# Kernel tuning notes

Measured on AMD Instinct MI355X. Metric: run time of the kernel, lower is better.

The kernel has to match this reference:

```python
import jax, jax.numpy as jnp
import numpy as np

D_MODEL = 1024
NUM_HEADS = 16
D_HEAD = D_MODEL // NUM_HEADS
NEG_INF = float(np.finfo(np.float32).min)


def setup_inputs() -> dict:
    key = jax.random.key(0)
    ks = jax.random.split(key, 6)
    B, S = 2, 2048
    q = jax.random.normal(ks[0], (B, S, D_MODEL), dtype=jnp.float32)
    k = jax.random.normal(ks[1], (B, S, D_MODEL), dtype=jnp.float32)
    v = jax.random.normal(ks[2], (B, S, D_MODEL), dtype=jnp.float32)
    # causal boolean mask: True = attend
    attn_mask = jnp.tril(jnp.ones((S, S), dtype=bool))
    # nn.Linear(d_model, d_model, bias=False) weights: [out, in]; y = x @ W.T
    init_scale = 1.0 / np.sqrt(D_MODEL)
    Wq = jax.random.uniform(ks[3], (D_MODEL, D_MODEL), jnp.float32, -init_scale, init_scale)
    Wk = jax.random.uniform(ks[4], (D_MODEL, D_MODEL), jnp.float32, -init_scale, init_scale)
    Wv = jax.random.uniform(ks[5], (D_MODEL, D_MODEL), jnp.float32, -init_scale, init_scale)
    return {"query": q, "key": k, "value": v, "Wq": Wq, "Wk": Wk, "Wv": Wv,
            "attn_mask": attn_mask}


def _split_heads(x):
    # [B, S, D_MODEL] -> [B, H, S, d_head]
    B, S, _ = x.shape
    return x.reshape(B, S, NUM_HEADS, D_HEAD).transpose(0, 2, 1, 3)


def reference(query, key, value, Wq, Wk, Wv, attn_mask):
    B, Sq, _ = query.shape
    Sk = key.shape[1]
    q = _split_heads(query @ Wq.T)   # [B, H, Sq, dh]
    k = _split_heads(key @ Wk.T)     # [B, H, Sk, dh]
    v = _split_heads(value @ Wv.T)   # [B, H, Sk, dh]
    scale = 1.0 / np.sqrt(D_HEAD)
    scores = jnp.einsum('bhqd,bhkd->bhqk', q, k) * scale  # [B, H, Sq, Sk]
    scores = jnp.where(attn_mask[None, None, :, :], scores, NEG_INF)
    attn_weights = jax.nn.softmax(scores, axis=-1)
    ctx = jnp.einsum('bhqk,bhkd->bhqd', attn_weights, v)   # [B, H, Sq, dh]
    context = ctx.transpose(0, 2, 1, 3).reshape(B, Sq, D_MODEL)
    return context, attn_weights
```

## Files before the change

kernel.cpp:

```cpp
#include <hip/hip_runtime.h>
#include <hip/hip_bf16.h>

#define B_ 2
#define H_ 16
#define S_ 2048
#define DH_ 64
#define DM_ 1024
#define BH_ (B_*H_)
#define CTX_ELEMS (B_*S_*DM_)
#define ATTNW_ELEMS ((size_t)BH_*S_*S_)
#define OUT_ELEMS ((size_t)CTX_ELEMS + ATTNW_ELEMS)
#define HEAD_ELEMS (S_*DH_)
#define XB_ELEMS ((size_t)3*B_*S_*DM_)

typedef __attribute__((ext_vector_type(4))) float  f32x4;
typedef __attribute__((ext_vector_type(8))) short  short8;
typedef __attribute__((ext_vector_type(4))) unsigned short ush4;
typedef unsigned short u16;
typedef unsigned int u32;

__device__ __forceinline__ u16 f2bf(float f) {
  union { __hip_bfloat16 h; u16 u; } cv;
  cv.h = __float2bfloat16(f);
  return cv.u;
}
__device__ __forceinline__ float bf2f(u16 u) {
  union { unsigned int i; float f; } cv;
  cv.i = ((unsigned int)u) << 16;
  return cv.f;
}

__device__ __forceinline__ void gload_lds16(const u16* g, u16* l) {
  __builtin_amdgcn_global_load_lds(
      (const __attribute__((address_space(1))) u32*)g,
      (__attribute__((address_space(3))) u32*)l, 16, 0, 0);
}

__global__ __launch_bounds__(256) void convert_all(
    const float* __restrict__ q, const float* __restrict__ k, const float* __restrict__ v,
    const float* __restrict__ wq, const float* __restrict__ wk, const float* __restrict__ wv,
    u16* __restrict__ xb, u16* __restrict__ wb)
{
  const int t = blockIdx.y;
  const float* s; u16* d; int nblk;
  if (t < 3) {
    s = (t == 0) ? wq : (t == 1) ? wk : wv;
    d = wb + (size_t)t * (DM_ * DM_);
    nblk = 512;
  } else {
    s = (t == 3) ? q : (t == 4) ? k : v;
    d = xb + (size_t)(t - 3) * ((size_t)B_ * S_ * DM_);
    nblk = 2048;
  }
  if (blockIdx.x >= nblk) return;
  const int i = (blockIdx.x * 256 + threadIdx.x) * 8;
  f32x4 a = *(const f32x4*)(s + i);
  f32x4 b = *(const f32x4*)(s + i + 4);
  short8 p;
#pragma unroll
  for (int j = 0; j < 4; ++j) { p[j] = (short)f2bf(a[j]); p[4 + j] = (short)f2bf(b[j]); }
  *(short8*)(d + i) = p;
}

__global__ __launch_bounds__(256) void proj_gemm(
    const u16* __restrict__ Xb, const u16* __restrict__ Wb,
    u16* __restrict__ qb, u16* __restrict__ kb, u16* __restrict__ vt,
    float* __restrict__ attnw)
{
  const u16* A = Xb + (size_t)blockIdx.z * ((size_t)B_ * S_ * DM_);
  const u16* W = Wb + (size_t)blockIdx.z * (DM_ * DM_);

  const int m0 = blockIdx.x * 128;
  const int n0 = blockIdx.y * 128;

  __shared__ u16 As[128 * 32];
  __shared__ u16 Bs[128 * 32];

  const int tid  = threadIdx.x;
  const int lane = tid & 63;
  const int w    = tid >> 6;
  const int wr   = w >> 1, wc = w & 1;
  const int l15  = lane & 15, l4 = lane >> 4;

  f32x4 acc[4][4];
#pragma unroll
  for (int i = 0; i < 4; ++i)
#pragma unroll
    for (int j = 0; j < 4; ++j) acc[i][j] = (f32x4){0.f, 0.f, 0.f, 0.f};

  const int srow = lane >> 2;
  const int scol = (lane & 3) * 8;
  const int ca = w * 2;
  const u16* ga0 = A + (size_t)(m0 + ca * 16 + srow) * DM_ + scol;
  const u16* ga1 = A + (size_t)(m0 + ca * 16 + 16 + srow) * DM_ + scol;
  const u16* gb0 = W + (size_t)(n0 + ca * 16 + srow) * DM_ + scol;
  const u16* gb1 = W + (size_t)(n0 + ca * 16 + 16 + srow) * DM_ + scol;

  for (int kb = 0; kb < DM_ / 32; ++kb) {
    const int k0 = kb * 32;
    gload_lds16(ga0 + k0, &As[ca * 512]);
    gload_lds16(ga1 + k0, &As[ca * 512 + 512]);
    gload_lds16(gb0 + k0, &Bs[ca * 512]);
    gload_lds16(gb1 + k0, &Bs[ca * 512 + 512]);
    __syncthreads();
    short8 af[4], bfr[4];
#pragma unroll
    for (int i = 0; i < 4; ++i)
      af[i] = *(const short8*)&As[(wr * 64 + i * 16 + l15) * 32 + l4 * 8];
#pragma unroll
    for (int j = 0; j < 4; ++j)
      bfr[j] = *(const short8*)&Bs[(wc * 64 + j * 16 + l15) * 32 + l4 * 8];
#pragma unroll
    for (int i = 0; i < 4; ++i)
#pragma unroll
      for (int j = 0; j < 4; ++j)
        acc[i][j] = __builtin_amdgcn_mfma_f32_16x16x32_bf16(af[i], bfr[j], acc[i][j], 0, 0, 0);
    __syncthreads();
  }

  if (blockIdx.z == 2) {
#pragma unroll
    for (int i = 0; i < 4; ++i)
#pragma unroll
      for (int j = 0; j < 4; ++j)
#pragma unroll
        for (int r = 0; r < 4; ++r) {
          const int grow = m0 + wr * 64 + i * 16 + l4 * 4 + r;
          const int gcol = n0 + wc * 64 + j * 16 + l15;
          const int b = grow >> 11, s = grow & (S_ - 1);
          const int h = gcol >> 6,  d = gcol & (DH_ - 1);
          vt[(size_t)((b << 4) + h) * HEAD_ELEMS + (size_t)d * S_ + s] = f2bf(acc[i][j][r]);
        }
  } else {
    u16* O = (blockIdx.z == 0) ? qb : kb;
#pragma unroll
    for (int i = 0; i < 4; ++i)
#pragma unroll
      for (int j = 0; j < 4; ++j)
#pragma unroll
        for (int r = 0; r < 4; ++r) {
          const int grow = m0 + wr * 64 + i * 16 + l4 * 4 + r;
          const int gcol = n0 + wc * 64 + j * 16 + l15;
          const int b = grow >> 11, s = grow & (S_ - 1);
          const int h = gcol >> 6,  d = gcol & (DH_ - 1);
          O[(size_t)((b << 4) + h) * HEAD_ELEMS + (size_t)s * DH_ + d] = f2bf(acc[i][j][r]);
        }
  }

  {
    const int p = (blockIdx.z * 8 + blockIdx.y) * 32 + blockIdx.x;
    const f32x4 z = (f32x4){0.f, 0.f, 0.f, 0.f};
    const int base = p * 60;
    for (int rr = 0; rr < 60; ++rr) {
      const int zrow = base + rr;
      const int bh = zrow / 1536;
      const int s  = zrow - bh * 1536;
      const int nc = ((s >> 7) + 1) << 7;
      float* orow = attnw + (size_t)bh * ((size_t)S_ * S_) + (size_t)s * S_;
      for (int c = nc + tid * 4; c < S_; c += 1024)
        __builtin_nontemporal_store(z, (f32x4*)(orow + c));
    }
  }
}

#define PROW 2048
#define ATT_SMEM (16 * PROW * 2 + 16 * 4 + 64 * 4)

__global__ __launch_bounds__(256) void attn_kernel(
    const u16* __restrict__ qb, const u16* __restrict__ kb, const u16* __restrict__ vt,
    float* __restrict__ ctx, float* __restrict__ attnw)
{
  extern __shared__ u16 smem[];
  u16* P = smem;
  float* rinv    = (float*)(smem + 16 * PROW);
  float* partial = rinv + 16;

  const int lin = blockIdx.y * 128 + blockIdx.x;
  const int nl  = (lin & 7) * 512 + (lin >> 3);
  const int bh  = nl >> 7;
  const int qtl = nl & 127;
  const int qt  = 127 - qtl;

  const int tid = threadIdx.x;
  const int lane = tid & 63;
  const int w = tid >> 6;
  const int l15 = lane & 15, l4 = lane >> 4;

  const int NCC = ((qt * 16 + 16) + 127) >> 7;
  const int ncols = NCC << 7;
  const int qtmax = qt * 16 + 15;

  const u16* Qb = qb + (size_t)bh * HEAD_ELEMS + (size_t)(qt * 16) * DH_;
  const u16* Kb = kb + (size_t)bh * HEAD_ELEMS;
  const u16* Vt = vt + (size_t)bh * HEAD_ELEMS;

  {
    short8 aQ0 = *(const short8*)(Qb + (size_t)l15 * DH_ + l4 * 8);
    short8 aQ1 = *(const short8*)(Qb + (size_t)l15 * DH_ + l4 * 8 + 32);
    const int qrow = l4 * 4;
    const int qabs = qt * 16 + qrow;
    float psum[4] = {0.f, 0.f, 0.f, 0.f};
    for (int ci = 0; ci < NCC; ++ci) {
      const int col0 = (ci << 7) + w * 32;
#pragma unroll
      for (int t = 0; t < 2; ++t) {
        const int ct = col0 + t * 16;
        const int cg = ct + l15;
        if (ct <= qtmax) {
          const u16* kp = Kb + (size_t)cg * DH_ + l4 * 8;
          short8 b0 = *(const short8*)(kp);
          short8 b1 = *(const short8*)(kp + 32);
          f32x4 a0 = (f32x4){0.f, 0.f, 0.f, 0.f};
          f32x4 a1 = (f32x4){0.f, 0.f, 0.f, 0.f};
          a0 = __builtin_amdgcn_mfma_f32_16x16x32_bf16(aQ0, b0, a0, 0, 0, 0);
          a1 = __builtin_amdgcn_mfma_f32_16x16x32_bf16(aQ1, b1, a1, 0, 0, 0);
          const f32x4 a = a0 + a1;
#pragma unroll
          for (int r = 0; r < 4; ++r) {
            const float e = (cg <= qabs + r) ? __expf(a[r] * 0.125f) : 0.f;
            psum[r] += e;
            const int row = qrow + r;
            P[(row << 11) + (cg ^ ((row & 7) << 3))] = f2bf(e);
          }
        } else {
#pragma unroll
          for (int r = 0; r < 4; ++r) {
            const int row = qrow + r;
            P[(row << 11) + (cg ^ ((row & 7) << 3))] = 0;
          }
        }
      }
    }
#pragma unroll
    for (int r = 0; r < 4; ++r) {
      float s = psum[r];
      s += __shfl_xor(s, 1);
      s += __shfl_xor(s, 2);
      s += __shfl_xor(s, 4);
      s += __shfl_xor(s, 8);
      if (l15 == 0) partial[w * 16 + qrow + r] = s;
    }
  }
  __syncthreads();
  if (tid < 16) {
    const float l = partial[tid] + partial[16 + tid] + partial[32 + tid] + partial[48 + tid];
    rinv[tid] = 1.0f / l;
  }
  __syncthreads();

  auto phase2a = [&]() {
    const bool do_zeros = (bh >= 30) || (qt >= 96);
    const f32x4 z = (f32x4){0.f, 0.f, 0.f, 0.f};
#pragma unroll
    for (int rr = 0; rr < 4; ++rr) {
      const int row = rr * 4 + w;
      const float inv = rinv[row];
      const int swz = (row & 7) << 3;
      const u16* prow = P + (row << 11);
      float* orow = attnw + (size_t)bh * ((size_t)S_ * S_) + (size_t)(qt * 16 + row) * S_;
      for (int c = lane * 4; c < ncols; c += 256) {
        ush4 pv = *(const ush4*)(prow + (c ^ swz));
        f32x4 o;
        o[0] = bf2f(pv[0]) * inv;
        o[1] = bf2f(pv[1]) * inv;
        o[2] = bf2f(pv[2]) * inv;
        o[3] = bf2f(pv[3]) * inv;
        __builtin_nontemporal_store(o, (f32x4*)(orow + c));
      }
      if (do_zeros) {
        for (int c = ncols + lane * 4; c < S_; c += 256)
          __builtin_nontemporal_store(z, (f32x4*)(orow + c));
      }
    }
  };

  auto phase2b = [&]() {
    const int dq = w;
    f32x4 acc0 = (f32x4){0.f, 0.f, 0.f, 0.f};
    f32x4 acc1 = (f32x4){0.f, 0.f, 0.f, 0.f};
    const u16* vp0 = Vt + (size_t)(dq * 16 + l15) * S_ + l4 * 8;
    const u16* prow = P + (l15 << 11);
    const int swz = (l15 & 7) << 3;
    for (int c = 0; c < ncols; c += 64) {
      short8 ap0 = *(const short8*)(prow + ((c + l4 * 8) ^ swz));
      short8 bv0 = *(const short8*)(vp0 + c);
      acc0 = __builtin_amdgcn_mfma_f32_16x16x32_bf16(ap0, bv0, acc0, 0, 0, 0);
      short8 ap1 = *(const short8*)(prow + ((c + 32 + l4 * 8) ^ swz));
      short8 bv1 = *(const short8*)(vp0 + c + 32);
      acc1 = __builtin_amdgcn_mfma_f32_16x16x32_bf16(ap1, bv1, acc1, 0, 0, 0);
    }
    const f32x4 acc = acc0 + acc1;
    const int b = bh >> 4, h = bh & 15;
#pragma unroll
    for (int r = 0; r < 4; ++r) {
      const int rg = qt * 16 + l4 * 4 + r;
      const float inv = rinv[l4 * 4 + r];
      __builtin_nontemporal_store(acc[r] * inv,
          ctx + (size_t)(b * S_ + rg) * DM_ + h * 64 + dq * 16 + l15);
    }
  };

  if (qtl & 1) { phase2b(); phase2a(); }
  else         { phase2a(); phase2b(); }
}

extern "C" void kernel_launch(void* const* d_in, const int* in_sizes, int n_in,
                              void* d_out, int out_size, void* d_ws, size_t ws_size,
                              hipStream_t stream) {
  const float* q  = (const float*)d_in[0];
  const float* k  = (const float*)d_in[1];
  const float* v  = (const float*)d_in[2];
  const float* Wq = (const float*)d_in[3];
  const float* Wk = (const float*)d_in[4];
  const float* Wv = (const float*)d_in[5];

  float* ctx   = (float*)d_out;
  float* attnw = ctx + CTX_ELEMS;

  u16* wb = (u16*)d_ws;
  u16* qb = wb + (size_t)3 * DM_ * DM_;
  u16* kb = qb + (size_t)BH_ * HEAD_ELEMS;
  u16* vt = kb + (size_t)BH_ * HEAD_ELEMS;
  u16* xb = (u16*)(ctx + (OUT_ELEMS - XB_ELEMS / 2));

  hipFuncSetAttribute(reinterpret_cast<const void*>(attn_kernel),
                      hipFuncAttributeMaxDynamicSharedMemorySize, ATT_SMEM);

  convert_all<<<dim3(2048, 6), 256, 0, stream>>>(q, k, v, Wq, Wk, Wv, xb, wb);
  proj_gemm<<<dim3(32, 8, 3), 256, 0, stream>>>(xb, wb, qb, kb, vt, attnw);
  attn_kernel<<<dim3(128, 32), 256, ATT_SMEM, stream>>>(qb, kb, vt, ctx, attnw);
}
```

Baseline: 247.4 us.

## Fuse attention-weight writes and zero-fill into the PV MFMA loop

```diff
diff --git a/kernel.cpp b/kernel.cpp
--- a/kernel.cpp
+++ b/kernel.cpp
@@ -64,8 +64,7 @@
 
 __global__ __launch_bounds__(256) void proj_gemm(
     const u16* __restrict__ Xb, const u16* __restrict__ Wb,
-    u16* __restrict__ qb, u16* __restrict__ kb, u16* __restrict__ vt,
-    float* __restrict__ attnw)
+    u16* __restrict__ qb, u16* __restrict__ kb, u16* __restrict__ vt)
 {
   const u16* A = Xb + (size_t)blockIdx.z * ((size_t)B_ * S_ * DM_);
   const u16* W = Wb + (size_t)blockIdx.z * (DM_ * DM_);
@@ -145,21 +144,6 @@
           const int h = gcol >> 6,  d = gcol & (DH_ - 1);
           O[(size_t)((b << 4) + h) * HEAD_ELEMS + (size_t)s * DH_ + d] = f2bf(acc[i][j][r]);
         }
-  }
-
-  {
-    const int p = (blockIdx.z * 8 + blockIdx.y) * 32 + blockIdx.x;
-    const f32x4 z = (f32x4){0.f, 0.f, 0.f, 0.f};
-    const int base = p * 60;
-    for (int rr = 0; rr < 60; ++rr) {
-      const int zrow = base + rr;
-      const int bh = zrow / 1536;
-      const int s  = zrow - bh * 1536;
-      const int nc = ((s >> 7) + 1) << 7;
-      float* orow = attnw + (size_t)bh * ((size_t)S_ * S_) + (size_t)s * S_;
-      for (int c = nc + tid * 4; c < S_; c += 1024)
-        __builtin_nontemporal_store(z, (f32x4*)(orow + c));
-    }
   }
 }
 
@@ -248,47 +232,38 @@
   }
   __syncthreads();
 
-  auto phase2a = [&]() {
-    const bool do_zeros = (bh >= 30) || (qt >= 96);
-    const f32x4 z = (f32x4){0.f, 0.f, 0.f, 0.f};
-#pragma unroll
-    for (int rr = 0; rr < 4; ++rr) {
-      const int row = rr * 4 + w;
-      const float inv = rinv[row];
-      const int swz = (row & 7) << 3;
-      const u16* prow = P + (row << 11);
-      float* orow = attnw + (size_t)bh * ((size_t)S_ * S_) + (size_t)(qt * 16 + row) * S_;
-      for (int c = lane * 4; c < ncols; c += 256) {
-        ush4 pv = *(const ush4*)(prow + (c ^ swz));
-        f32x4 o;
-        o[0] = bf2f(pv[0]) * inv;
-        o[1] = bf2f(pv[1]) * inv;
-        o[2] = bf2f(pv[2]) * inv;
-        o[3] = bf2f(pv[3]) * inv;
-        __builtin_nontemporal_store(o, (f32x4*)(orow + c));
-      }
-      if (do_zeros) {
-        for (int c = ncols + lane * 4; c < S_; c += 256)
-          __builtin_nontemporal_store(z, (f32x4*)(orow + c));
-      }
-    }
-  };
-
-  auto phase2b = [&]() {
-    const int dq = w;
+  {
     f32x4 acc0 = (f32x4){0.f, 0.f, 0.f, 0.f};
     f32x4 acc1 = (f32x4){0.f, 0.f, 0.f, 0.f};
-    const u16* vp0 = Vt + (size_t)(dq * 16 + l15) * S_ + l4 * 8;
-    const u16* prow = P + (l15 << 11);
-    const int swz = (l15 & 7) << 3;
-    for (int c = 0; c < ncols; c += 64) {
-      short8 ap0 = *(const short8*)(prow + ((c + l4 * 8) ^ swz));
+    const u16* vp0 = Vt + (size_t)(w * 16 + l15) * S_ + l4 * 8;
+    const u16* ppv = P + (l15 << 11);
+    const int swpv = (l15 & 7) << 3;
+    const int row2a = w + l4 * 4;
+    const float inv2a = rinv[row2a];
+    const u16* p2a = P + (row2a << 11);
+    const int sw2a = (row2a & 7) << 3;
+    float* orow = attnw + (size_t)bh * ((size_t)S_ * S_) + (size_t)(qt * 16 + row2a) * S_;
+    const f32x4 z = (f32x4){0.f, 0.f, 0.f, 0.f};
+
+    int c = 0;
+    for (; c < ncols; c += 64) {
+      short8 ap0 = *(const short8*)(ppv + ((c + l4 * 8) ^ swpv));
       short8 bv0 = *(const short8*)(vp0 + c);
       acc0 = __builtin_amdgcn_mfma_f32_16x16x32_bf16(ap0, bv0, acc0, 0, 0, 0);
-      short8 ap1 = *(const short8*)(prow + ((c + 32 + l4 * 8) ^ swz));
+      ush4 pv = *(const ush4*)(p2a + ((c + l15 * 4) ^ sw2a));
+      short8 ap1 = *(const short8*)(ppv + ((c + 32 + l4 * 8) ^ swpv));
       short8 bv1 = *(const short8*)(vp0 + c + 32);
       acc1 = __builtin_amdgcn_mfma_f32_16x16x32_bf16(ap1, bv1, acc1, 0, 0, 0);
+      f32x4 o;
+      o[0] = bf2f(pv[0]) * inv2a;
+      o[1] = bf2f(pv[1]) * inv2a;
+      o[2] = bf2f(pv[2]) * inv2a;
+      o[3] = bf2f(pv[3]) * inv2a;
+      __builtin_nontemporal_store(o, (f32x4*)(orow + c + l15 * 4));
     }
+    for (; c < S_; c += 64)
+      __builtin_nontemporal_store(z, (f32x4*)(orow + c + l15 * 4));
+
     const f32x4 acc = acc0 + acc1;
     const int b = bh >> 4, h = bh & 15;
 #pragma unroll
@@ -296,12 +271,9 @@
       const int rg = qt * 16 + l4 * 4 + r;
       const float inv = rinv[l4 * 4 + r];
       __builtin_nontemporal_store(acc[r] * inv,
-          ctx + (size_t)(b * S_ + rg) * DM_ + h * 64 + dq * 16 + l15);
+          ctx + (size_t)(b * S_ + rg) * DM_ + h * 64 + w * 16 + l15);
     }
-  };
-
-  if (qtl & 1) { phase2b(); phase2a(); }
-  else         { phase2a(); phase2b(); }
+  }
 }
 
 extern "C" void kernel_launch(void* const* d_in, const int* in_sizes, int n_in,
@@ -327,6 +299,6 @@
                       hipFuncAttributeMaxDynamicSharedMemorySize, ATT_SMEM);
 
   convert_all<<<dim3(2048, 6), 256, 0, stream>>>(q, k, v, Wq, Wk, Wv, xb, wb);
-  proj_gemm<<<dim3(32, 8, 3), 256, 0, stream>>>(xb, wb, qb, kb, vt, attnw);
+  proj_gemm<<<dim3(32, 8, 3), 256, 0, stream>>>(xb, wb, qb, kb, vt);
   attn_kernel<<<dim3(128, 32), 256, ATT_SMEM, stream>>>(qb, kb, vt, ctx, attnw);
 }
```

After: 232.9 us. -5.9%, faster.
